# Kernel tuning notes

Measured on AMD Instinct MI355X. Metric: run time of the kernel, lower is better.

## Reference

```python
import jax, jax.numpy as jnp
import numpy as np

NODES = 50000
E = 800000
META = 4
IN_DIM = 512
NHID = 128
C = 2
WEIGHT_DECAY = 5e-4
BN_EPS = 1e-3


def setup_inputs() -> dict:
    key = jax.random.key(0)
    ks = jax.random.split(key, 12)
    x = jax.random.normal(ks[0], (NODES, IN_DIM), dtype=jnp.float32) * 0.1
    # glorot-uniform style init
    W1 = jax.random.uniform(ks[1], (IN_DIM, NHID), minval=-1.0, maxval=1.0) * np.sqrt(6.0 / (IN_DIM + NHID))
    W2 = jax.random.uniform(ks[2], (NHID, C), minval=-1.0, maxval=1.0) * np.sqrt(6.0 / (NHID + C))
    w_omega = jax.random.normal(ks[3], (NODES * C, META), dtype=jnp.float32) * 0.01
    b_omega = jax.random.normal(ks[4], (META,), dtype=jnp.float32) * 0.01
    u_omega = jax.random.normal(ks[5], (META,), dtype=jnp.float32) * 0.01
    sup_rows = jax.random.randint(ks[6], (META, E), 0, NODES, dtype=jnp.int32)
    sup_cols = jax.random.randint(ks[7], (META, E), 0, NODES, dtype=jnp.int32)
    # positive values mimicking a normalized adjacency
    sup_vals = jax.random.uniform(ks[8], (META, E), dtype=jnp.float32) / 16.0
    label = jax.nn.one_hot(jax.random.randint(ks[9], (NODES,), 0, C), C, dtype=jnp.float32)
    mask = (jax.random.uniform(ks[10], (NODES,)) < 0.2).astype(jnp.float32)
    return {"x": x, "W1": W1, "W2": W2, "w_omega": w_omega, "b_omega": b_omega,
            "u_omega": u_omega, "sup_rows": sup_rows, "sup_cols": sup_cols,
            "sup_vals": sup_vals, "label": label, "mask": mask}


def _spmm(rows, cols, vals, h, n):
    # COO sparse @ dense: out[r] += v * h[c]
    return jax.ops.segment_sum(vals[:, None] * h[cols], rows, num_segments=n)


def reference(x, W1, W2, w_omega, b_omega, u_omega, sup_rows, sup_cols, sup_vals, label, mask):
    n = x.shape[0]
    # Layer 1: x @ W1 is shared across meta-paths (same GCN weights)
    pre1 = x @ W1  # [n, nhid]
    spmm_shared = jax.vmap(lambda r, c, v: _spmm(r, c, v, pre1, n))
    h1 = spmm_shared(sup_rows, sup_cols, sup_vals)  # [META, n, nhid]
    # tf.nn.batch_normalization over node axis, no scale/offset, eps=1e-3, then relu
    mean = h1.mean(axis=1, keepdims=True)
    var = h1.var(axis=1, keepdims=True)
    h1 = jax.nn.relu((h1 - mean) * jax.lax.rsqrt(var + BN_EPS))
    # Layer 2: per-meta-path pre_sup then sparse propagation, no norm, identity act
    pre2 = h1 @ W2  # [META, n, C]
    h2 = jax.vmap(lambda r, c, v, h: _spmm(r, c, v, h, n))(sup_rows, sup_cols, sup_vals, pre2)
    # Attention fusion over meta-paths (HAN-style)
    flat = h2.reshape(h2.shape[0], n * h2.shape[2])  # [META, n*C]
    v = jnp.tanh(flat @ w_omega + b_omega)           # [META, META]
    alphas = jax.nn.softmax(v @ u_omega)             # [META]
    logits = (flat * alphas[:, None]).sum(0).reshape(n, -1)  # [n, C]
    # L2 reg on trainable vars + masked softmax cross-entropy
    l2 = (0.5 * jnp.sum(W1 * W1) + 0.5 * jnp.sum(W2 * W2) + 0.5 * jnp.sum(w_omega * w_omega)
          + 0.5 * jnp.sum(b_omega * b_omega) + 0.5 * jnp.sum(u_omega * u_omega))
    maskf = mask / jnp.mean(mask)
    ce = jnp.mean(-jnp.sum(label * jax.nn.log_softmax(logits), axis=1) * maskf)
    loss = WEIGHT_DECAY * l2 + ce
    acc = jnp.mean((jnp.argmax(logits, 1) == jnp.argmax(label, 1)).astype(jnp.float32) * maskf)
    return loss, acc
```

## Files before the change

### kernel.cpp

```cpp
#include <hip/hip_runtime.h>
#include <hip/hip_bf16.h>
#include <math.h>

#define N_NODES 50000
#define EDGES   800000
#define META    4
#define IN_DIM  512
#define NHID    128
#define NCLS    2
#define TOT_ROWS  (META * N_NODES)
#define TOT_EDGES (META * EDGES)
#define RPB    256
#define NBKT   196
#define NBKT_TOT (META * NBKT)
#define EPB    2048
#define NSLICE ((EDGES + EPB - 1) / EPB)
#define BKTCAP 5120

typedef __bf16 bf16x8 __attribute__((ext_vector_type(8)));
typedef float  f32x4  __attribute__((ext_vector_type(4)));
typedef int    i32x2  __attribute__((ext_vector_type(2)));
typedef int    i32x4  __attribute__((ext_vector_type(4)));

__device__ __forceinline__ float bfbits_lo(unsigned int p) {
  return __uint_as_float((p & 0xFFFFu) << 16);
}
__device__ __forceinline__ float bfbits_hi(unsigned int p) {
  return __uint_as_float(p & 0xFFFF0000u);
}
__device__ __forceinline__ unsigned int pack_bf16x2(float a, float b) {
  __bf16 ba = (__bf16)a, bb = (__bf16)b;
  return ((unsigned int)__builtin_bit_cast(unsigned short, bb) << 16) |
         (unsigned int)__builtin_bit_cast(unsigned short, ba);
}

__global__ __launch_bounds__(256) void pack_w1(const float* __restrict__ W1,
                                               __bf16* __restrict__ Wh,
                                               __bf16* __restrict__ Wl) {
  int idx = blockIdx.x * 256 + threadIdx.x;
  if (idx >= 16 * 8 * 64) return;
  int l = idx & 63, st = idx >> 6, t = st & 7, s = st >> 3;
  int col = t * 16 + (l & 15);
  int k0 = s * 32 + (l >> 4) * 8;
#pragma unroll
  for (int i = 0; i < 8; ++i) {
    float w = W1[(size_t)(k0 + i) * NHID + col];
    __bf16 h = (__bf16)w;
    Wh[(size_t)idx * 8 + i] = h;
    Wl[(size_t)idx * 8 + i] = (__bf16)(w - (float)h);
  }
}

__global__ __launch_bounds__(256) void gemm_mfma(const float* __restrict__ X,
                                                 const __bf16* __restrict__ Wh,
                                                 const __bf16* __restrict__ Wl,
                                                 __bf16* __restrict__ C) {
  int w = threadIdx.x >> 6, l = threadIdx.x & 63;
  int lrow = l & 15, lk = l >> 4;
  int row = blockIdx.x * 64 + w * 16 + lrow;
  int rowc = row < N_NODES ? row : N_NODES - 1;
  f32x4 acc[8] = {};
  const bf16x8* whv = (const bf16x8*)Wh;
  const bf16x8* wlv = (const bf16x8*)Wl;

  for (int s = 0; s < 16; ++s) {
    const float* ap = &X[(size_t)rowc * IN_DIM + s * 32 + lk * 8];
    float4 a0 = *reinterpret_cast<const float4*>(ap);
    float4 a1 = *reinterpret_cast<const float4*>(ap + 4);
    float av[8] = {a0.x, a0.y, a0.z, a0.w, a1.x, a1.y, a1.z, a1.w};
    bf16x8 ah, al;
#pragma unroll
    for (int i = 0; i < 8; ++i) {
      float v = av[i];
      __bf16 h = (__bf16)v;
      ah[i] = h;
      al[i] = (__bf16)(v - (float)h);
    }
    int fbase = (s * 8) * 64 + l;
#pragma unroll
    for (int t = 0; t < 8; ++t) {
      bf16x8 bh = whv[fbase + t * 64];
      bf16x8 bl = wlv[fbase + t * 64];
      acc[t] = __builtin_amdgcn_mfma_f32_16x16x32_bf16(ah, bh, acc[t], 0, 0, 0);
      acc[t] = __builtin_amdgcn_mfma_f32_16x16x32_bf16(ah, bl, acc[t], 0, 0, 0);
      acc[t] = __builtin_amdgcn_mfma_f32_16x16x32_bf16(al, bh, acc[t], 0, 0, 0);
    }
  }
  int crow0 = blockIdx.x * 64 + w * 16 + lk * 4;
#pragma unroll
  for (int t = 0; t < 8; ++t) {
    int col = t * 16 + lrow;
#pragma unroll
    for (int r = 0; r < 4; ++r) {
      int crow = crow0 + r;
      if (crow < N_NODES) C[(size_t)crow * NHID + col] = (__bf16)acc[t][r];
    }
  }
}

__global__ __launch_bounds__(256) void bin_lds(const int* __restrict__ rows,
                                               const int* __restrict__ cols,
                                               const float* __restrict__ vals,
                                               int2* __restrict__ frontier,
                                               int* __restrict__ bcnt) {
  __shared__ int2 stg[EPB];
  __shared__ int  dst[EPB];
  __shared__ int  cnt[256];
  __shared__ int  scn[256];
  __shared__ int  gbase[256];
  __shared__ int  lcur[256];
  int tid = threadIdx.x;
  int m = blockIdx.y, slice = blockIdx.x;
  int e0 = slice * EPB;
  int n = EDGES - e0; n = n < EPB ? n : EPB;

  cnt[tid] = 0;
  __syncthreads();

  int r_[8], c_[8]; float v_[8];
#pragma unroll
  for (int k = 0; k < 8; ++k) {
    int i = k * 256 + tid;
    if (i < n) {
      size_t e = (size_t)m * EDGES + e0 + i;
      r_[k] = __builtin_nontemporal_load(&rows[e]);
      c_[k] = __builtin_nontemporal_load(&cols[e]);
      v_[k] = __builtin_nontemporal_load(&vals[e]);
      atomicAdd(&cnt[r_[k] >> 8], 1);
    } else {
      r_[k] = -1;
    }
  }
  __syncthreads();

  int own = cnt[tid];
  scn[tid] = own;
  __syncthreads();
  for (int off = 1; off < 256; off <<= 1) {
    int add = (tid >= off) ? scn[tid - off] : 0;
    __syncthreads();
    scn[tid] += add;
    __syncthreads();
  }
  int excl = scn[tid] - own;
  scn[tid] = excl;
  if (tid < NBKT && own > 0)
    gbase[tid] = (m * NBKT + tid) * BKTCAP + atomicAdd(&bcnt[m * NBKT + tid], own);
  lcur[tid] = 0;
  __syncthreads();

#pragma unroll
  for (int k = 0; k < 8; ++k) {
    if (r_[k] >= 0) {
      int bkt = r_[k] >> 8;
      int lp = atomicAdd(&lcur[bkt], 1);
      int s = scn[bkt] + lp;
      int2 ed;
      ed.x = ((r_[k] & (RPB - 1)) << 16) | c_[k];
      ed.y = __float_as_int(v_[k]);
      stg[s] = ed;
      dst[s] = gbase[bkt] + lp;
    }
  }
  __syncthreads();

  for (int i = tid; i < n; i += 256)
    frontier[dst[i]] = stg[i];
}

__global__ __launch_bounds__(1024) void bucket_scan(const int* __restrict__ bcnt,
                                                    int* __restrict__ bucket_base,
                                                    int* __restrict__ row_ptr) {
  __shared__ int lds[1024];
  int t = threadIdx.x;
  int total = (t < NBKT_TOT) ? bcnt[t] : 0;
  lds[t] = total;
  __syncthreads();
  for (int off = 1; off < 1024; off <<= 1) {
    int add = (t >= off) ? lds[t - off] : 0;
    __syncthreads();
    lds[t] += add;
    __syncthreads();
  }
  if (t < NBKT_TOT) bucket_base[t] = lds[t] - total;
  if (t == NBKT_TOT - 1) row_ptr[TOT_ROWS] = lds[t];
}

__global__ __launch_bounds__(256) void bucket_csr(const int2* __restrict__ frontier,
                                                  const int* __restrict__ bcnt,
                                                  const int* __restrict__ bucket_base,
                                                  int* __restrict__ row_ptr,
                                                  int2* __restrict__ csr_ed) {
  __shared__ int cnt[256];
  __shared__ int scn[256];
  int tid = threadIdx.x;
  int m = blockIdx.y, bkt = blockIdx.x;
  int n = bcnt[m * NBKT + bkt];
  const int2* seg = &frontier[(size_t)(m * NBKT + bkt) * BKTCAP];
  cnt[tid] = 0;
  __syncthreads();
  for (int j = tid; j < n; j += 256)
    atomicAdd(&cnt[seg[j].x >> 16], 1);
  __syncthreads();
  int v = cnt[tid];
  scn[tid] = v;
  __syncthreads();
  for (int off = 1; off < 256; off <<= 1) {
    int add = (tid >= off) ? scn[tid - off] : 0;
    __syncthreads();
    scn[tid] += add;
    __syncthreads();
  }
  int base = bucket_base[m * NBKT + bkt];
  int excl = base + scn[tid] - v;
  int row = bkt * RPB + tid;
  if (row < N_NODES) row_ptr[m * N_NODES + row] = excl;
  __syncthreads();
  cnt[tid] = excl;
  __syncthreads();
  for (int j = tid; j < n; j += 256) {
    int2 ed = seg[j];
    int pos = atomicAdd(&cnt[ed.x >> 16], 1);
    int2 o;
    o.x = ed.x & 0xFFFF;
    o.y = ed.y;
    csr_ed[pos] = o;
  }
}

__global__ __launch_bounds__(256) void gather1_all(const int* __restrict__ row_ptr,
                                                   const int2* __restrict__ csr_ed,
                                                   const int4* __restrict__ pre1q,
                                                   int4* __restrict__ h1q,
                                                   float* __restrict__ stats) {
  __shared__ float lsum[4][16][8];
  __shared__ float lsq[4][16][8];
  int tid = threadIdx.x;
  int wv = tid >> 6, lane = tid & 63;
  int g = lane >> 4, l16 = lane & 15;
  int mm = blockIdx.y;
  int r = blockIdx.x * 16 + wv * 4 + g;
  int gr = mm * N_NODES + r;
  int start = row_ptr[gr];
  int len = row_ptr[gr + 1] - start;

  float acc[8] = {};
  int jb = 0;
  for (; jb + 8 <= len; jb += 8) {
#pragma unroll
    for (int k = 0; k < 8; ++k) {
      i32x2 ed = __builtin_nontemporal_load((const i32x2*)&csr_ed[start + jb + k]);
      float v = __int_as_float(ed.y);
      int4 p = pre1q[(size_t)ed.x * 16 + l16];
      acc[0] = fmaf(v, bfbits_lo((unsigned)p.x), acc[0]);
      acc[1] = fmaf(v, bfbits_hi((unsigned)p.x), acc[1]);
      acc[2] = fmaf(v, bfbits_lo((unsigned)p.y), acc[2]);
      acc[3] = fmaf(v, bfbits_hi((unsigned)p.y), acc[3]);
      acc[4] = fmaf(v, bfbits_lo((unsigned)p.z), acc[4]);
      acc[5] = fmaf(v, bfbits_hi((unsigned)p.z), acc[5]);
      acc[6] = fmaf(v, bfbits_lo((unsigned)p.w), acc[6]);
      acc[7] = fmaf(v, bfbits_hi((unsigned)p.w), acc[7]);
    }
  }
  if (jb < len) {
#pragma unroll
    for (int k = 0; k < 8; ++k) {
      int idx = jb + k;
      int j = idx < len ? start + idx : start;
      float msk = idx < len ? 1.0f : 0.0f;
      i32x2 ed = __builtin_nontemporal_load((const i32x2*)&csr_ed[j]);
      float v = msk * __int_as_float(ed.y);
      int4 p = pre1q[(size_t)ed.x * 16 + l16];
      acc[0] = fmaf(v, bfbits_lo((unsigned)p.x), acc[0]);
      acc[1] = fmaf(v, bfbits_hi((unsigned)p.x), acc[1]);
      acc[2] = fmaf(v, bfbits_lo((unsigned)p.y), acc[2]);
      acc[3] = fmaf(v, bfbits_hi((unsigned)p.y), acc[3]);
      acc[4] = fmaf(v, bfbits_lo((unsigned)p.z), acc[4]);
      acc[5] = fmaf(v, bfbits_hi((unsigned)p.z), acc[5]);
      acc[6] = fmaf(v, bfbits_lo((unsigned)p.w), acc[6]);
      acc[7] = fmaf(v, bfbits_hi((unsigned)p.w), acc[7]);
    }
  }

  i32x4 ho;
  ho.x = (int)pack_bf16x2(acc[0], acc[1]);
  ho.y = (int)pack_bf16x2(acc[2], acc[3]);
  ho.z = (int)pack_bf16x2(acc[4], acc[5]);
  ho.w = (int)pack_bf16x2(acc[6], acc[7]);
  __builtin_nontemporal_store(ho, (i32x4*)&h1q[(size_t)gr * 16 + l16]);

  float sq[8];
#pragma unroll
  for (int i = 0; i < 8; ++i) sq[i] = acc[i] * acc[i];
#pragma unroll
  for (int i = 0; i < 8; ++i) {
    acc[i] += __shfl_xor(acc[i], 16);
    acc[i] += __shfl_xor(acc[i], 32);
    sq[i]  += __shfl_xor(sq[i], 16);
    sq[i]  += __shfl_xor(sq[i], 32);
  }
  if (g == 0) {
#pragma unroll
    for (int i = 0; i < 8; ++i) {
      lsum[wv][l16][i] = acc[i];
      lsq[wv][l16][i]  = sq[i];
    }
  }
  __syncthreads();
  if (tid < 128) {
    int a = tid >> 3, b = tid & 7;
    float s = lsum[0][a][b] + lsum[1][a][b] + lsum[2][a][b] + lsum[3][a][b];
    float q = lsq[0][a][b] + lsq[1][a][b] + lsq[2][a][b] + lsq[3][a][b];
    atomicAdd(&stats[mm * 256 + tid], s);
    atomicAdd(&stats[mm * 256 + 128 + tid], q);
  }
}

__global__ __launch_bounds__(256) void bn_apply_all(const int4* __restrict__ h1q,
                                                    const float* __restrict__ stats,
                                                    const float* __restrict__ W2,
                                                    float* __restrict__ pre2) {
  int tid = threadIdx.x;
  int wv = tid >> 6, lane = tid & 63;
  int g = lane >> 4, l16 = lane & 15;
  int mm = blockIdx.y;
  int n = blockIdx.x * 16 + wv * 4 + g;
  const float inv_n = 1.0f / (float)N_NODES;
  const float* st = stats + mm * 256;
  int4 p = h1q[((size_t)mm * N_NODES + n) * 16 + l16];
  unsigned int pw[4] = {(unsigned)p.x, (unsigned)p.y, (unsigned)p.z, (unsigned)p.w};
  float c0 = 0.f, c1 = 0.f;
#pragma unroll
  for (int i = 0; i < 8; ++i) {
    int h = l16 * 8 + i;
    float xv = (i & 1) ? bfbits_hi(pw[i >> 1]) : bfbits_lo(pw[i >> 1]);
    float mean = st[h] * inv_n;
    float var = st[128 + h] * inv_n - mean * mean;
    float rs = rsqrtf(var + 1e-3f);
    float y = (xv - mean) * rs;
    y = y > 0.f ? y : 0.f;
    c0 = fmaf(y, W2[h * 2 + 0], c0);
    c1 = fmaf(y, W2[h * 2 + 1], c1);
  }
#pragma unroll
  for (int off = 1; off < 16; off <<= 1) {
    c0 += __shfl_xor(c0, off);
    c1 += __shfl_xor(c1, off);
  }
  if (l16 == 0) {
    pre2[((size_t)mm * N_NODES + n) * 2 + 0] = c0;
    pre2[((size_t)mm * N_NODES + n) * 2 + 1] = c1;
  }
}

__global__ __launch_bounds__(256) void gather2_all(const int* __restrict__ row_ptr,
                                                   const int2* __restrict__ csr_ed,
                                                   const float* __restrict__ pre2,
                                                   float* __restrict__ h2) {
  int r = blockIdx.x * 256 + threadIdx.x;
  int m = blockIdx.y;
  if (r >= N_NODES) return;
  int start = row_ptr[m * N_NODES + r];
  int len = row_ptr[m * N_NODES + r + 1] - start;
  const float2* p2 = (const float2*)(pre2 + (size_t)m * N_NODES * 2);
  float a0 = 0.f, a1 = 0.f;
  int jb = 0;
  for (; jb + 8 <= len; jb += 8) {
#pragma unroll
    for (int k = 0; k < 8; ++k) {
      i32x2 ed = __builtin_nontemporal_load((const i32x2*)&csr_ed[start + jb + k]);
      float v = __int_as_float(ed.y);
      float2 p = p2[ed.x];
      a0 = fmaf(v, p.x, a0);
      a1 = fmaf(v, p.y, a1);
    }
  }
  if (jb < len) {
#pragma unroll
    for (int k = 0; k < 8; ++k) {
      int idx = jb + k;
      int j = idx < len ? start + idx : start;
      float msk = idx < len ? 1.0f : 0.0f;
      i32x2 ed = __builtin_nontemporal_load((const i32x2*)&csr_ed[j]);
      float v = msk * __int_as_float(ed.y);
      float2 p = p2[ed.x];
      a0 = fmaf(v, p.x, a0);
      a1 = fmaf(v, p.y, a1);
    }
  }
  h2[((size_t)m * N_NODES + r) * 2 + 0] = a0;
  h2[((size_t)m * N_NODES + r) * 2 + 1] = a1;
}

__global__ __launch_bounds__(256) void att_dot_kernel(const float* __restrict__ h2,
                                                      const float* __restrict__ w_omega,
                                                      float* __restrict__ vacc) {
  float acc[16] = {};
  int stride = gridDim.x * blockDim.x;
  for (int i = blockIdx.x * blockDim.x + threadIdx.x; i < N_NODES * NCLS; i += stride) {
    float4 w = *reinterpret_cast<const float4*>(&w_omega[(size_t)i * 4]);
#pragma unroll
    for (int m = 0; m < 4; ++m) {
      float f = h2[(size_t)m * (N_NODES * NCLS) + i];
      acc[m * 4 + 0] = fmaf(f, w.x, acc[m * 4 + 0]);
      acc[m * 4 + 1] = fmaf(f, w.y, acc[m * 4 + 1]);
      acc[m * 4 + 2] = fmaf(f, w.z, acc[m * 4 + 2]);
      acc[m * 4 + 3] = fmaf(f, w.w, acc[m * 4 + 3]);
    }
  }
#pragma unroll
  for (int q = 0; q < 16; ++q) {
    float v = acc[q];
    for (int off = 32; off; off >>= 1) v += __shfl_down(v, off);
    if ((threadIdx.x & 63) == 0) atomicAdd(&vacc[q], v);
  }
}

__global__ void att_final_kernel(const float* __restrict__ vacc,
                                 const float* __restrict__ b_omega,
                                 const float* __restrict__ u_omega,
                                 float* __restrict__ alphas) {
  if (threadIdx.x == 0 && blockIdx.x == 0) {
    float s[4];
    for (int m = 0; m < 4; ++m) {
      float sm = 0.f;
      for (int j = 0; j < 4; ++j)
        sm += tanhf(vacc[m * 4 + j] + b_omega[j]) * u_omega[j];
      s[m] = sm;
    }
    float mx = fmaxf(fmaxf(s[0], s[1]), fmaxf(s[2], s[3]));
    float ex[4], den = 0.f;
    for (int m = 0; m < 4; ++m) { ex[m] = expf(s[m] - mx); den += ex[m]; }
    for (int m = 0; m < 4; ++m) alphas[m] = ex[m] / den;
  }
}

#define SQ0 400000
#define SQ1 (SQ0 + 65536)
#define SQ2 (SQ1 + 256)
#define SQ3 (SQ2 + 4)
#define SQ4 (SQ3 + 4)
__global__ __launch_bounds__(256) void sumsq_all(const float* __restrict__ w_omega,
                                                 const float* __restrict__ W1,
                                                 const float* __restrict__ W2,
                                                 const float* __restrict__ b_omega,
                                                 const float* __restrict__ u_omega,
                                                 float* __restrict__ out) {
  float s = 0.f;
  int stride = gridDim.x * blockDim.x;
  for (int i = blockIdx.x * blockDim.x + threadIdx.x; i < SQ4; i += stride) {
    float v;
    if (i < SQ0) v = w_omega[i];
    else if (i < SQ1) v = W1[i - SQ0];
    else if (i < SQ2) v = W2[i - SQ1];
    else if (i < SQ3) v = b_omega[i - SQ2];
    else v = u_omega[i - SQ3];
    s = fmaf(v, v, s);
  }
  for (int off = 32; off; off >>= 1) s += __shfl_down(s, off);
  if ((threadIdx.x & 63) == 0) atomicAdd(out, s);
}

__global__ __launch_bounds__(256) void loss_kernel(const float* __restrict__ h2,
                                                   const float* __restrict__ alphas,
                                                   const float* __restrict__ label,
                                                   const float* __restrict__ mask,
                                                   float* __restrict__ scal) {
  int n = blockIdx.x * blockDim.x + threadIdx.x;
  float msum = 0.f, cesum = 0.f, accsum = 0.f;
  if (n < N_NODES) {
    float a0 = alphas[0], a1 = alphas[1], a2 = alphas[2], a3 = alphas[3];
    const int S = N_NODES * NCLS;
    float l0 = a0 * h2[n * 2] + a1 * h2[S + n * 2] + a2 * h2[2 * S + n * 2] + a3 * h2[3 * S + n * 2];
    float l1 = a0 * h2[n * 2 + 1] + a1 * h2[S + n * 2 + 1] + a2 * h2[2 * S + n * 2 + 1] + a3 * h2[3 * S + n * 2 + 1];
    float mx = fmaxf(l0, l1);
    float lse = mx + logf(expf(l0 - mx) + expf(l1 - mx));
    float lb0 = label[n * 2], lb1 = label[n * 2 + 1];
    float ce = -(lb0 * (l0 - lse) + lb1 * (l1 - lse));
    int pred = (l1 > l0) ? 1 : 0;
    int larg = (lb1 > lb0) ? 1 : 0;
    float corr = (pred == larg) ? 1.f : 0.f;
    float mk = mask[n];
    msum = mk;
    cesum = ce * mk;
    accsum = corr * mk;
  }
  for (int off = 32; off; off >>= 1) {
    msum += __shfl_down(msum, off);
    cesum += __shfl_down(cesum, off);
    accsum += __shfl_down(accsum, off);
  }
  if ((threadIdx.x & 63) == 0) {
    atomicAdd(&scal[0], msum);
    atomicAdd(&scal[1], cesum);
    atomicAdd(&scal[2], accsum);
  }
}

__global__ void final_kernel(const float* __restrict__ scal, float* __restrict__ out) {
  if (threadIdx.x == 0 && blockIdx.x == 0) {
    out[0] = 5e-4f * 0.5f * scal[3] + scal[1] / scal[0];
    out[1] = scal[2] / scal[0];
  }
}

extern "C" void kernel_launch(void* const* d_in, const int* in_sizes, int n_in,
                              void* d_out, int out_size, void* d_ws, size_t ws_size,
                              hipStream_t stream) {
  const float* x       = (const float*)d_in[0];
  const float* W1      = (const float*)d_in[1];
  const float* W2      = (const float*)d_in[2];
  const float* w_omega = (const float*)d_in[3];
  const float* b_omega = (const float*)d_in[4];
  const float* u_omega = (const float*)d_in[5];
  const int*   sup_rows = (const int*)d_in[6];
  const int*   sup_cols = (const int*)d_in[7];
  const float* sup_vals = (const float*)d_in[8];
  const float* label   = (const float*)d_in[9];
  const float* mask    = (const float*)d_in[10];
  float* out = (float*)d_out;

  float* ws = (float*)d_ws;
  __bf16* pre1b   = (__bf16*)ws;
  float*  pre2    = ws + 3200000;
  float*  h2      = ws + 3600000;
  int2*   csr_ed  = (int2*)(ws + 4000000);
  int*    row_ptr = (int*)(ws + 10400000);
  int*    bcnt    = (int*)(ws + 10600016);
  int*    bbase   = (int*)(ws + 10601024);
  float*  stats   = ws + 10602048;
  float*  scal    = ws + 10603072;
  float*  vacc    = ws + 10603080;
  float*  alphas  = ws + 10603096;
  __bf16* Wh      = (__bf16*)(ws + 10603100);
  __bf16* Wl      = (__bf16*)(ws + 10635868);
  int2*   frontier = (int2*)(ws + 11000000);
  int4*   h1q      = (int4*)(ws + 11000000);

  pack_w1<<<dim3(32), dim3(256), 0, stream>>>(W1, Wh, Wl);
  gemm_mfma<<<dim3(782), dim3(256), 0, stream>>>(x, Wh, Wl, pre1b);

  hipMemsetAsync(bcnt, 0, NBKT_TOT * sizeof(int), stream);
  hipMemsetAsync(stats, 0, (1024 + 8 + 16) * sizeof(float), stream);

  bin_lds<<<dim3(NSLICE, META), dim3(256), 0, stream>>>(
      sup_rows, sup_cols, sup_vals, frontier, bcnt);
  bucket_scan<<<dim3(1), dim3(1024), 0, stream>>>(bcnt, bbase, row_ptr);
  bucket_csr<<<dim3(NBKT, META), dim3(256), 0, stream>>>(frontier, bcnt, bbase,
                                                         row_ptr, csr_ed);

  gather1_all<<<dim3(3125, META), dim3(256), 0, stream>>>(
      row_ptr, csr_ed, (const int4*)pre1b, h1q, stats);

  bn_apply_all<<<dim3(3125, META), dim3(256), 0, stream>>>(h1q, stats, W2, pre2);

  gather2_all<<<dim3(196, META), dim3(256), 0, stream>>>(row_ptr, csr_ed, pre2, h2);

  att_dot_kernel<<<dim3(64), dim3(256), 0, stream>>>(h2, w_omega, vacc);
  att_final_kernel<<<dim3(1), dim3(64), 0, stream>>>(vacc, b_omega, u_omega, alphas);

  sumsq_all<<<dim3(128), dim3(256), 0, stream>>>(w_omega, W1, W2, b_omega, u_omega, scal + 3);

  loss_kernel<<<dim3(196), dim3(256), 0, stream>>>(h2, alphas, label, mask, scal);
  final_kernel<<<dim3(1), dim3(64), 0, stream>>>(scal, out);
}
```

Before: 496.8 us.

## Drop split-bf16 GEMM compensation, register-cache bucket edges, merge workspace memsets

```diff
diff --git a/kernel.cpp b/kernel.cpp
--- a/kernel.cpp
+++ b/kernel.cpp
@@ -16,6 +16,7 @@
 #define EPB    2048
 #define NSLICE ((EDGES + EPB - 1) / EPB)
 #define BKTCAP 5120
+#define REG_E  20
 
 typedef __bf16 bf16x8 __attribute__((ext_vector_type(8)));
 typedef float  f32x4  __attribute__((ext_vector_type(4)));
@@ -35,25 +36,19 @@
 }
 
 __global__ __launch_bounds__(256) void pack_w1(const float* __restrict__ W1,
-                                               __bf16* __restrict__ Wh,
-                                               __bf16* __restrict__ Wl) {
+                                               __bf16* __restrict__ Wh) {
   int idx = blockIdx.x * 256 + threadIdx.x;
   if (idx >= 16 * 8 * 64) return;
   int l = idx & 63, st = idx >> 6, t = st & 7, s = st >> 3;
   int col = t * 16 + (l & 15);
   int k0 = s * 32 + (l >> 4) * 8;
 #pragma unroll
-  for (int i = 0; i < 8; ++i) {
-    float w = W1[(size_t)(k0 + i) * NHID + col];
-    __bf16 h = (__bf16)w;
-    Wh[(size_t)idx * 8 + i] = h;
-    Wl[(size_t)idx * 8 + i] = (__bf16)(w - (float)h);
-  }
+  for (int i = 0; i < 8; ++i)
+    Wh[(size_t)idx * 8 + i] = (__bf16)W1[(size_t)(k0 + i) * NHID + col];
 }
 
 __global__ __launch_bounds__(256) void gemm_mfma(const float* __restrict__ X,
                                                  const __bf16* __restrict__ Wh,
-                                                 const __bf16* __restrict__ Wl,
                                                  __bf16* __restrict__ C) {
   int w = threadIdx.x >> 6, l = threadIdx.x & 63;
   int lrow = l & 15, lk = l >> 4;
@@ -61,29 +56,19 @@
   int rowc = row < N_NODES ? row : N_NODES - 1;
   f32x4 acc[8] = {};
   const bf16x8* whv = (const bf16x8*)Wh;
-  const bf16x8* wlv = (const bf16x8*)Wl;
 
   for (int s = 0; s < 16; ++s) {
     const float* ap = &X[(size_t)rowc * IN_DIM + s * 32 + lk * 8];
     float4 a0 = *reinterpret_cast<const float4*>(ap);
     float4 a1 = *reinterpret_cast<const float4*>(ap + 4);
-    float av[8] = {a0.x, a0.y, a0.z, a0.w, a1.x, a1.y, a1.z, a1.w};
-    bf16x8 ah, al;
-#pragma unroll
-    for (int i = 0; i < 8; ++i) {
-      float v = av[i];
-      __bf16 h = (__bf16)v;
-      ah[i] = h;
-      al[i] = (__bf16)(v - (float)h);
-    }
+    bf16x8 ah;
+    ah[0] = (__bf16)a0.x; ah[1] = (__bf16)a0.y; ah[2] = (__bf16)a0.z; ah[3] = (__bf16)a0.w;
+    ah[4] = (__bf16)a1.x; ah[5] = (__bf16)a1.y; ah[6] = (__bf16)a1.z; ah[7] = (__bf16)a1.w;
     int fbase = (s * 8) * 64 + l;
 #pragma unroll
     for (int t = 0; t < 8; ++t) {
       bf16x8 bh = whv[fbase + t * 64];
-      bf16x8 bl = wlv[fbase + t * 64];
       acc[t] = __builtin_amdgcn_mfma_f32_16x16x32_bf16(ah, bh, acc[t], 0, 0, 0);
-      acc[t] = __builtin_amdgcn_mfma_f32_16x16x32_bf16(ah, bl, acc[t], 0, 0, 0);
-      acc[t] = __builtin_amdgcn_mfma_f32_16x16x32_bf16(al, bh, acc[t], 0, 0, 0);
     }
   }
   int crow0 = blockIdx.x * 64 + w * 16 + lk * 4;
@@ -196,12 +181,24 @@
   int tid = threadIdx.x;
   int m = blockIdx.y, bkt = blockIdx.x;
   int n = bcnt[m * NBKT + bkt];
-  const int2* seg = &frontier[(size_t)(m * NBKT + bkt) * BKTCAP];
+  n = n < BKTCAP ? n : BKTCAP;
+  const i32x2* seg = (const i32x2*)&frontier[(size_t)(m * NBKT + bkt) * BKTCAP];
+
+  i32x2 ed_[REG_E];
+#pragma unroll
+  for (int k = 0; k < REG_E; ++k) {
+    int j = k * 256 + tid;
+    if (j < n) ed_[k] = __builtin_nontemporal_load(&seg[j]);
+    else       ed_[k].x = -1;
+  }
+
   cnt[tid] = 0;
   __syncthreads();
-  for (int j = tid; j < n; j += 256)
-    atomicAdd(&cnt[seg[j].x >> 16], 1);
-  __syncthreads();
+#pragma unroll
+  for (int k = 0; k < REG_E; ++k)
+    if (ed_[k].x >= 0) atomicAdd(&cnt[ed_[k].x >> 16], 1);
+  __syncthreads();
+
   int v = cnt[tid];
   scn[tid] = v;
   __syncthreads();
@@ -218,13 +215,15 @@
   __syncthreads();
   cnt[tid] = excl;
   __syncthreads();
-  for (int j = tid; j < n; j += 256) {
-    int2 ed = seg[j];
-    int pos = atomicAdd(&cnt[ed.x >> 16], 1);
-    int2 o;
-    o.x = ed.x & 0xFFFF;
-    o.y = ed.y;
-    csr_ed[pos] = o;
+#pragma unroll
+  for (int k = 0; k < REG_E; ++k) {
+    if (ed_[k].x >= 0) {
+      int pos = atomicAdd(&cnt[ed_[k].x >> 16], 1);
+      int2 o;
+      o.x = ed_[k].x & 0xFFFF;
+      o.y = ed_[k].y;
+      csr_ed[pos] = o;
+    }
   }
 }
 
@@ -527,21 +526,19 @@
   int2*   csr_ed  = (int2*)(ws + 4000000);
   int*    row_ptr = (int*)(ws + 10400000);
   int*    bcnt    = (int*)(ws + 10600016);
-  int*    bbase   = (int*)(ws + 10601024);
-  float*  stats   = ws + 10602048;
-  float*  scal    = ws + 10603072;
-  float*  vacc    = ws + 10603080;
-  float*  alphas  = ws + 10603096;
-  __bf16* Wh      = (__bf16*)(ws + 10603100);
-  __bf16* Wl      = (__bf16*)(ws + 10635868);
+  float*  stats   = ws + 10600800;
+  float*  scal    = ws + 10601824;
+  float*  vacc    = ws + 10601832;
+  float*  alphas  = ws + 10601848;
+  int*    bbase   = (int*)(ws + 10601852);
+  __bf16* Wh      = (__bf16*)(ws + 10602880);
   int2*   frontier = (int2*)(ws + 11000000);
   int4*   h1q      = (int4*)(ws + 11000000);
 
-  pack_w1<<<dim3(32), dim3(256), 0, stream>>>(W1, Wh, Wl);
-  gemm_mfma<<<dim3(782), dim3(256), 0, stream>>>(x, Wh, Wl, pre1b);
-
-  hipMemsetAsync(bcnt, 0, NBKT_TOT * sizeof(int), stream);
-  hipMemsetAsync(stats, 0, (1024 + 8 + 16) * sizeof(float), stream);
+  pack_w1<<<dim3(32), dim3(256), 0, stream>>>(W1, Wh);
+  gemm_mfma<<<dim3(782), dim3(256), 0, stream>>>(x, Wh, pre1b);
+
+  hipMemsetAsync(bcnt, 0, 1832 * sizeof(float), stream);
 
   bin_lds<<<dim3(NSLICE, META), dim3(256), 0, stream>>>(
       sup_rows, sup_cols, sup_vals, frontier, bcnt);
```

Result: faster. 482.1 us (-3.0%).
